# Kernel optimization log

Measured on AMD Instinct MI355X. Metric: run time of the kernel, lower is better.

The kernel has to match this reference:

```python
import jax, jax.numpy as jnp
import numpy as np
import math

B, M, C = 256, 256, 1024
ALPHA = 0.1

def setup_inputs() -> dict:
    key = jax.random.key(0)
    k1, k2 = jax.random.split(key)
    input_encoded = jax.random.normal(k1, (B, C), dtype=jnp.float32)
    memory_mean = jax.random.normal(k2, (M, C), dtype=jnp.float32)
    return {"input_encoded": input_encoded, "memory_mean": memory_mean}

def reference(input_encoded, memory_mean):
    b, c = input_encoded.shape
    m = memory_mean.shape[0]
    # ---- write_to_memory ----
    # similarity of each input with each prior memory slot: [B, M]
    sims = jnp.einsum('bc,mc->bm', input_encoded, memory_mean)
    closest_idx = jnp.argmax(sims, axis=1)                      # [B]
    sel = memory_mean[closest_idx]                              # [B, C]
    new_row = (1.0 - ALPHA) * sel + ALPHA * input_encoded       # [B, C]
    onehot = (jnp.arange(m)[None, :] == closest_idx[:, None])   # [B, M] bool
    mem = jnp.broadcast_to(memory_mean[None], (b, m, c))
    updated_memory = jnp.where(onehot[:, :, None], new_row[:, None, :], mem)  # [B, M, C]
    dkl_write = 0.5 * jnp.sum((input_encoded - sel) ** 2, axis=1)             # [B]
    # ---- read_with_encoded_input ----
    scale = 1.0 / math.sqrt(c)
    scores = jnp.einsum('bc,bmc->bm', input_encoded, updated_memory) * scale  # [B, M]
    attn = jax.nn.softmax(scores, axis=1)
    z_read = jnp.einsum('bm,bmc->bc', attn, updated_memory)                   # [B, C]
    dkl_read = 0.5 * jnp.sum((z_read - input_encoded) ** 2, axis=1)           # [B]
    kl_div = dkl_write + dkl_read
    return z_read, updated_memory, kl_div
```

## Files before the change

### kernel.cpp

```cpp
#include <hip/hip_runtime.h>
#include <math.h>

#define B_DIM 256
#define M_DIM 256
#define C_DIM 1024
#define C4    256
#define UM_OFF (B_DIM * C_DIM)
#define KL_OFF (UM_OFF + B_DIM * M_DIM * C_DIM)
#define SCALE  0.03125f

__device__ __forceinline__ float dot4(float4 a, float4 b) {
    return a.x*b.x + a.y*b.y + a.z*b.z + a.w*b.w;
}
__device__ __forceinline__ float wsum(float v) {
    #pragma unroll
    for (int off = 32; off; off >>= 1) v += __shfl_xor(v, off, 64);
    return v;
}
__device__ __forceinline__ float wmax(float v) {
    #pragma unroll
    for (int off = 32; off; off >>= 1) v = fmaxf(v, __shfl_xor(v, off, 64));
    return v;
}
__device__ __forceinline__ float4 blend9(float4 v, float4 xr) {
    return make_float4(0.9f*v.x + 0.1f*xr.x, 0.9f*v.y + 0.1f*xr.y,
                       0.9f*v.z + 0.1f*xr.z, 0.9f*v.w + 0.1f*xr.w);
}

__global__ __launch_bounds__(256) void tm_stream(const float* __restrict__ x,
                                                 const float* __restrict__ mem,
                                                 float* __restrict__ out) {
    const int j = blockIdx.x;
    const int b  = j >> 5;
    const int m0 = (j & 31) << 3;
    const int t = threadIdx.x;
    const int lane = t & 63;
    const int wv = t >> 6;

    __shared__ float s_p[8][4];

    const float4* src = (const float4*)mem + (m0 << 8) + t;
    float4 r0 = src[0 << 8];
    float4 r1 = src[1 << 8];
    float4 r2 = src[2 << 8];
    float4 r3 = src[3 << 8];
    float4 r4 = src[4 << 8];
    float4 r5 = src[5 << 8];
    float4 r6 = src[6 << 8];
    float4 r7 = src[7 << 8];
    const float4 xv = ((const float4*)(x + (size_t)b * C_DIM))[t];

    float p0 = dot4(r0, xv), p1 = dot4(r1, xv), p2 = dot4(r2, xv), p3 = dot4(r3, xv);
    float p4 = dot4(r4, xv), p5 = dot4(r5, xv), p6 = dot4(r6, xv), p7 = dot4(r7, xv);
    p0 = wsum(p0); p1 = wsum(p1); p2 = wsum(p2); p3 = wsum(p3);
    p4 = wsum(p4); p5 = wsum(p5); p6 = wsum(p6); p7 = wsum(p7);
    if (lane == 0) {
        s_p[0][wv] = p0; s_p[1][wv] = p1; s_p[2][wv] = p2; s_p[3][wv] = p3;
        s_p[4][wv] = p4; s_p[5][wv] = p5; s_p[6][wv] = p6; s_p[7][wv] = p7;
    }
    __syncthreads();
    if (t < 8)
        out[(size_t)b * C_DIM + m0 + t] = s_p[t][0] + s_p[t][1] + s_p[t][2] + s_p[t][3];

    float4* dst = (float4*)(out + UM_OFF) + ((size_t)b << 16) + (m0 << 8) + t;
    dst[0 << 8] = r0;
    dst[1 << 8] = r1;
    dst[2 << 8] = r2;
    dst[3 << 8] = r3;
    dst[4 << 8] = r4;
    dst[5 << 8] = r5;
    dst[6 << 8] = r6;
    dst[7 << 8] = r7;
}

__global__ __launch_bounds__(1024) void tm_post(const float* __restrict__ x,
                                                const float* __restrict__ mem,
                                                float* __restrict__ out) {
    const int b = blockIdx.x;
    const int t = threadIdx.x;
    const int lane = t & 63;
    const int wv = t >> 6;
    const int tc = t & 255;
    const int q  = t >> 8;

    __shared__ float4 s_x[C4];
    __shared__ float4 s_zp[3][C4];
    __shared__ float  s_w[4];

    const float4* mem4 = (const float4*)mem;

    float4 xv = make_float4(0.f, 0.f, 0.f, 0.f);
    if (q == 0) {
        xv = ((const float4*)(x + (size_t)b * C_DIM))[tc];
        s_x[tc] = xv;
    }
    __syncthreads();

    const float* simsrow = out + (size_t)b * C_DIM;
    const float v0 = simsrow[lane];
    const float v1 = simsrow[lane + 64];
    const float v2 = simsrow[lane + 128];
    const float v3 = simsrow[lane + 192];
    const float4 xa = s_x[lane], xb = s_x[lane + 64];
    const float4 xc = s_x[lane + 128], xd = s_x[lane + 192];
    const float n2 = wsum(dot4(xa,xa) + dot4(xb,xb) + dot4(xc,xc) + dot4(xd,xd));

    float av = v0; int am = lane;
    if (v1 > av) { av = v1; am = lane + 64; }
    if (v2 > av) { av = v2; am = lane + 128; }
    if (v3 > av) { av = v3; am = lane + 192; }
    #pragma unroll
    for (int off = 32; off; off >>= 1) {
        float ov = __shfl_xor(av, off, 64);
        int   oi = __shfl_xor(am, off, 64);
        if (ov > av || (ov == av && oi < am)) { av = ov; am = oi; }
    }
    const int idx = am;
    const float fused = 0.9f * av + 0.1f * n2;

    float s0 = ((lane      ) == idx ? fused : v0) * SCALE;
    float s1 = ((lane +  64) == idx ? fused : v1) * SCALE;
    float s2 = ((lane + 128) == idx ? fused : v2) * SCALE;
    float s3 = ((lane + 192) == idx ? fused : v3) * SCALE;
    const float mx = wmax(fmaxf(fmaxf(s0, s1), fmaxf(s2, s3)));
    const float e0 = expf(s0 - mx), e1 = expf(s1 - mx);
    const float e2 = expf(s2 - mx), e3 = expf(s3 - mx);
    const float inv = 1.0f / wsum(e0 + e1 + e2 + e3);
    const float a0 = e0 * inv, a1 = e1 * inv, a2 = e2 * inv, a3 = e3 * inv;

    float aidx;
    if      (idx <  64) aidx = __shfl(a0, idx,       64);
    else if (idx < 128) aidx = __shfl(a1, idx - 64,  64);
    else if (idx < 192) aidx = __shfl(a2, idx - 128, 64);
    else                aidx = __shfl(a3, idx - 192, 64);
    aidx *= 0.1f;

    float dw = 0.f;
    if (wv == 0) {
        const float4* ir = mem4 + (idx << 8);
        float4 q0 = ir[lane], q1 = ir[lane+64], q2 = ir[lane+128], q3 = ir[lane+192];
        float p = 0.f; float4 dq;
        dq = make_float4(xa.x-q0.x, xa.y-q0.y, xa.z-q0.z, xa.w-q0.w); p += dot4(dq,dq);
        dq = make_float4(xb.x-q1.x, xb.y-q1.y, xb.z-q1.z, xb.w-q1.w); p += dot4(dq,dq);
        dq = make_float4(xc.x-q2.x, xc.y-q2.y, xc.z-q2.z, xc.w-q2.w); p += dot4(dq,dq);
        dq = make_float4(xd.x-q3.x, xd.y-q3.y, xd.z-q3.z, xd.w-q3.w); p += dot4(dq,dq);
        dw = wsum(p);
    }

    float4 z = make_float4(0.f, 0.f, 0.f, 0.f);
    {
        const float4* zsrc = mem4 + ((q << 6) << 8) + tc;
        auto zrun = [&](float areg) {
            #pragma unroll 4
            for (int i = 0; i < 64; ++i) {
                const float a = __shfl(areg, i, 64);
                float4 v = zsrc[i << 8];
                z.x = fmaf(a, v.x, z.x);
                z.y = fmaf(a, v.y, z.y);
                z.z = fmaf(a, v.z, z.z);
                z.w = fmaf(a, v.w, z.w);
            }
        };
        if      (q == 0) zrun(a0);
        else if (q == 1) zrun(a1);
        else if (q == 2) zrun(a2);
        else             zrun(a3);
    }
    if (q) s_zp[q - 1][tc] = z;
    __syncthreads();
    float drp = 0.f;
    if (q == 0) {
        float4 z1 = s_zp[0][tc], z2 = s_zp[1][tc], z3 = s_zp[2][tc];
        z.x += z1.x + z2.x + z3.x;
        z.y += z1.y + z2.y + z3.y;
        z.z += z1.z + z2.z + z3.z;
        z.w += z1.w + z2.w + z3.w;
        float4 sl = mem4[(idx << 8) + tc];
        float4 d = make_float4(xv.x - sl.x, xv.y - sl.y, xv.z - sl.z, xv.w - sl.w);
        z.x = fmaf(aidx, d.x, z.x);
        z.y = fmaf(aidx, d.y, z.y);
        z.z = fmaf(aidx, d.z, z.z);
        z.w = fmaf(aidx, d.w, z.w);
        float ex = z.x - xv.x, ey = z.y - xv.y, ez = z.z - xv.z, ew = z.w - xv.w;
        drp = ex*ex + ey*ey + ez*ez + ew*ew;
        ((float4*)out)[(size_t)b * C4 + tc] = z;
        ((float4*)(out + UM_OFF))[((size_t)b << 16) + (idx << 8) + tc] = blend9(sl, xv);
    }
    {
        float s = wsum(drp);
        if (q == 0 && lane == 0) s_w[wv] = s;
    }
    __syncthreads();
    if (t == 0) out[KL_OFF + b] = 0.5f * (dw + s_w[0] + s_w[1] + s_w[2] + s_w[3]);
}

extern "C" void kernel_launch(void* const* d_in, const int* in_sizes, int n_in,
                              void* d_out, int out_size, void* d_ws, size_t ws_size,
                              hipStream_t stream) {
    const float* x   = (const float*)d_in[0];
    const float* mem = (const float*)d_in[1];
    float* out = (float*)d_out;

    tm_stream<<<dim3(8192), dim3(256), 0, stream>>>(x, mem, out);
    tm_post<<<dim3(B_DIM), dim3(1024), 0, stream>>>(x, mem, out);
}
```

Before: 60.14 us.

## Split post kernel into batched attention-GEMV and finalize kernels sharing memory loads

Replaces the single per-batch post kernel with two kernels. The middle kernel processes four batch rows per block, so each loaded memory row is reused across four attention vectors. Its partial z sums go to scratch space inside the updated-memory output region, and idx, alpha and the write KL go to the workspace. A final kernel reduces the four partials, writes z and the KL term, and restores the overwritten memory rows plus the blended row. The aim is to cut redundant reads of the memory matrix in the read phase, at the cost of an extra launch and extra global round trips.

```diff
diff --git a/kernel.cpp b/kernel.cpp
--- a/kernel.cpp
+++ b/kernel.cpp
@@ -73,36 +73,31 @@
     dst[7 << 8] = r7;
 }
 
-__global__ __launch_bounds__(1024) void tm_post(const float* __restrict__ x,
-                                                const float* __restrict__ mem,
-                                                float* __restrict__ out) {
-    const int b = blockIdx.x;
+__global__ __launch_bounds__(256) void tm_mid(const float* __restrict__ x,
+                                              const float* __restrict__ mem,
+                                              float* __restrict__ out,
+                                              float* __restrict__ ws) {
+    const int blk = blockIdx.x;
+    const int gg = blk >> 2;
+    const int qq = blk & 3;
+    const int b0 = gg << 2;
     const int t = threadIdx.x;
     const int lane = t & 63;
-    const int wv = t >> 6;
-    const int tc = t & 255;
-    const int q  = t >> 8;
-
-    __shared__ float4 s_x[C4];
-    __shared__ float4 s_zp[3][C4];
-    __shared__ float  s_w[4];
+    const int j = t >> 6;
+    const int b = b0 + j;
+
+    __shared__ float s_attnT[64][4];
 
     const float4* mem4 = (const float4*)mem;
-
-    float4 xv = make_float4(0.f, 0.f, 0.f, 0.f);
-    if (q == 0) {
-        xv = ((const float4*)(x + (size_t)b * C_DIM))[tc];
-        s_x[tc] = xv;
-    }
-    __syncthreads();
 
     const float* simsrow = out + (size_t)b * C_DIM;
     const float v0 = simsrow[lane];
     const float v1 = simsrow[lane + 64];
     const float v2 = simsrow[lane + 128];
     const float v3 = simsrow[lane + 192];
-    const float4 xa = s_x[lane], xb = s_x[lane + 64];
-    const float4 xc = s_x[lane + 128], xd = s_x[lane + 192];
+    const float4* x4 = (const float4*)(x + (size_t)b * C_DIM);
+    const float4 xa = x4[lane], xb = x4[lane + 64];
+    const float4 xc = x4[lane + 128], xd = x4[lane + 192];
     const float n2 = wsum(dot4(xa,xa) + dot4(xb,xb) + dot4(xc,xc) + dot4(xd,xd));
 
     float av = v0; int am = lane;
@@ -128,15 +123,16 @@
     const float inv = 1.0f / wsum(e0 + e1 + e2 + e3);
     const float a0 = e0 * inv, a1 = e1 * inv, a2 = e2 * inv, a3 = e3 * inv;
 
-    float aidx;
-    if      (idx <  64) aidx = __shfl(a0, idx,       64);
-    else if (idx < 128) aidx = __shfl(a1, idx - 64,  64);
-    else if (idx < 192) aidx = __shfl(a2, idx - 128, 64);
-    else                aidx = __shfl(a3, idx - 192, 64);
-    aidx *= 0.1f;
-
-    float dw = 0.f;
-    if (wv == 0) {
+    const float aq = (qq == 0) ? a0 : (qq == 1) ? a1 : (qq == 2) ? a2 : a3;
+    s_attnT[lane][j] = aq;
+
+    if (qq == 0) {
+        float aidx;
+        if      (idx <  64) aidx = __shfl(a0, idx,       64);
+        else if (idx < 128) aidx = __shfl(a1, idx - 64,  64);
+        else if (idx < 192) aidx = __shfl(a2, idx - 128, 64);
+        else                aidx = __shfl(a3, idx - 192, 64);
+
         const float4* ir = mem4 + (idx << 8);
         float4 q0 = ir[lane], q1 = ir[lane+64], q2 = ir[lane+128], q3 = ir[lane+192];
         float p = 0.f; float4 dq;
@@ -144,54 +140,88 @@
         dq = make_float4(xb.x-q1.x, xb.y-q1.y, xb.z-q1.z, xb.w-q1.w); p += dot4(dq,dq);
         dq = make_float4(xc.x-q2.x, xc.y-q2.y, xc.z-q2.z, xc.w-q2.w); p += dot4(dq,dq);
         dq = make_float4(xd.x-q3.x, xd.y-q3.y, xd.z-q3.z, xd.w-q3.w); p += dot4(dq,dq);
-        dw = wsum(p);
-    }
-
-    float4 z = make_float4(0.f, 0.f, 0.f, 0.f);
-    {
-        const float4* zsrc = mem4 + ((q << 6) << 8) + tc;
-        auto zrun = [&](float areg) {
-            #pragma unroll 4
-            for (int i = 0; i < 64; ++i) {
-                const float a = __shfl(areg, i, 64);
-                float4 v = zsrc[i << 8];
-                z.x = fmaf(a, v.x, z.x);
-                z.y = fmaf(a, v.y, z.y);
-                z.z = fmaf(a, v.z, z.z);
-                z.w = fmaf(a, v.w, z.w);
-            }
-        };
-        if      (q == 0) zrun(a0);
-        else if (q == 1) zrun(a1);
-        else if (q == 2) zrun(a2);
-        else             zrun(a3);
-    }
-    if (q) s_zp[q - 1][tc] = z;
+        const float dwv = wsum(p);
+
+        if (lane == 0) {
+            ((int*)ws)[b]  = idx;
+            ws[256 + b] = aidx * 0.1f;
+            ws[512 + b] = dwv;
+        }
+    }
     __syncthreads();
-    float drp = 0.f;
-    if (q == 0) {
-        float4 z1 = s_zp[0][tc], z2 = s_zp[1][tc], z3 = s_zp[2][tc];
-        z.x += z1.x + z2.x + z3.x;
-        z.y += z1.y + z2.y + z3.y;
-        z.z += z1.z + z2.z + z3.z;
-        z.w += z1.w + z2.w + z3.w;
-        float4 sl = mem4[(idx << 8) + tc];
-        float4 d = make_float4(xv.x - sl.x, xv.y - sl.y, xv.z - sl.z, xv.w - sl.w);
-        z.x = fmaf(aidx, d.x, z.x);
-        z.y = fmaf(aidx, d.y, z.y);
-        z.z = fmaf(aidx, d.z, z.z);
-        z.w = fmaf(aidx, d.w, z.w);
-        float ex = z.x - xv.x, ey = z.y - xv.y, ez = z.z - xv.z, ew = z.w - xv.w;
-        drp = ex*ex + ey*ey + ez*ez + ew*ew;
-        ((float4*)out)[(size_t)b * C4 + tc] = z;
-        ((float4*)(out + UM_OFF))[((size_t)b << 16) + (idx << 8) + tc] = blend9(sl, xv);
-    }
-    {
-        float s = wsum(drp);
-        if (q == 0 && lane == 0) s_w[wv] = s;
-    }
+
+    float4 z0 = make_float4(0,0,0,0), z1 = z0, z2 = z0, z3 = z0;
+    const float4* src = mem4 + ((qq << 6) << 8) + t;
+    const float4* attn4 = (const float4*)s_attnT;
+    #pragma unroll 8
+    for (int i = 0; i < 64; ++i) {
+        float4 v = src[i << 8];
+        float4 a = attn4[i];
+        z0.x = fmaf(a.x, v.x, z0.x); z0.y = fmaf(a.x, v.y, z0.y);
+        z0.z = fmaf(a.x, v.z, z0.z); z0.w = fmaf(a.x, v.w, z0.w);
+        z1.x = fmaf(a.y, v.x, z1.x); z1.y = fmaf(a.y, v.y, z1.y);
+        z1.z = fmaf(a.y, v.z, z1.z); z1.w = fmaf(a.y, v.w, z1.w);
+        z2.x = fmaf(a.z, v.x, z2.x); z2.y = fmaf(a.z, v.y, z2.y);
+        z2.z = fmaf(a.z, v.z, z2.z); z2.w = fmaf(a.z, v.w, z2.w);
+        z3.x = fmaf(a.w, v.x, z3.x); z3.y = fmaf(a.w, v.y, z3.y);
+        z3.z = fmaf(a.w, v.z, z3.z); z3.w = fmaf(a.w, v.w, z3.w);
+    }
+    float4* umb = (float4*)(out + UM_OFF);
+    umb[((size_t)(b0 + 0) << 16) + (qq << 8) + t] = z0;
+    umb[((size_t)(b0 + 1) << 16) + (qq << 8) + t] = z1;
+    umb[((size_t)(b0 + 2) << 16) + (qq << 8) + t] = z2;
+    umb[((size_t)(b0 + 3) << 16) + (qq << 8) + t] = z3;
+}
+
+__global__ __launch_bounds__(256) void tm_fin(const float* __restrict__ x,
+                                              const float* __restrict__ mem,
+                                              float* __restrict__ out,
+                                              const float* __restrict__ ws) {
+    const int b = blockIdx.x;
+    const int t = threadIdx.x;
+    const int lane = t & 63;
+    const int wv = t >> 6;
+    __shared__ float s_w[4];
+
+    const int   idx  = ((const int*)ws)[b];
+    const float aidx = ws[256 + b];
+    const float dw   = ws[512 + b];
+
+    const float4* mem4 = (const float4*)mem;
+    float4* um = (float4*)(out + UM_OFF) + ((size_t)b << 16);
+
+    float4 p0 = um[(0 << 8) + t];
+    float4 p1 = um[(1 << 8) + t];
+    float4 p2 = um[(2 << 8) + t];
+    float4 p3 = um[(3 << 8) + t];
+    const float4 xv = ((const float4*)(x + (size_t)b * C_DIM))[t];
+    float4 sl = mem4[(idx << 8) + t];
+
+    float4 d = make_float4(xv.x - sl.x, xv.y - sl.y, xv.z - sl.z, xv.w - sl.w);
+    float4 z;
+    z.x = p0.x + p1.x + p2.x + p3.x + aidx * d.x;
+    z.y = p0.y + p1.y + p2.y + p3.y + aidx * d.y;
+    z.z = p0.z + p1.z + p2.z + p3.z + aidx * d.z;
+    z.w = p0.w + p1.w + p2.w + p3.w + aidx * d.w;
+
+    float ex = z.x - xv.x, ey = z.y - xv.y, ez = z.z - xv.z, ew = z.w - xv.w;
+    float drp = ex*ex + ey*ey + ez*ez + ew*ew;
+
+    ((float4*)out)[(size_t)b * C4 + t] = z;
+
+    #pragma unroll
+    for (int r = 0; r < 4; ++r) {
+        float4 v = mem4[(r << 8) + t];
+        if (idx == r) v = blend9(v, xv);
+        um[(r << 8) + t] = v;
+    }
+    if (idx >= 4) um[(idx << 8) + t] = blend9(sl, xv);
+
+    const float s = wsum(drp);
+    if (lane == 0) s_w[wv] = s;
     __syncthreads();
-    if (t == 0) out[KL_OFF + b] = 0.5f * (dw + s_w[0] + s_w[1] + s_w[2] + s_w[3]);
+    if (t == 0)
+        out[KL_OFF + b] = 0.5f * (dw + s_w[0] + s_w[1] + s_w[2] + s_w[3]);
 }
 
 extern "C" void kernel_launch(void* const* d_in, const int* in_sizes, int n_in,
@@ -200,7 +230,9 @@
     const float* x   = (const float*)d_in[0];
     const float* mem = (const float*)d_in[1];
     float* out = (float*)d_out;
+    float* ws  = (float*)d_ws;
 
     tm_stream<<<dim3(8192), dim3(256), 0, stream>>>(x, mem, out);
-    tm_post<<<dim3(B_DIM), dim3(1024), 0, stream>>>(x, mem, out);
-}
+    tm_mid<<<dim3(256), dim3(256), 0, stream>>>(x, mem, out, ws);
+    tm_fin<<<dim3(256), dim3(256), 0, stream>>>(x, mem, out, ws);
+}
```

Result: no change. 58.98 us (-1.9%).
